# Kernel optimization log

Measured on AMD Instinct MI355X. Metric: run time of the kernel, lower is better.

Reference implementation:

```python
import jax, jax.numpy as jnp
import numpy as np

BN_EPS = 1e-5
LN_EPS = 1e-5

N_NODES = 50000
N_EDGES = 800000
D_IN = 128
D_HID = 512


def _batchnorm(h, gamma, beta):
    # training-mode BatchNorm1d: biased variance over the node/batch dim
    m = jnp.mean(h, axis=0)
    v = jnp.mean(jnp.square(h - m), axis=0)
    return (h - m) * jax.lax.rsqrt(v + BN_EPS) * gamma + beta


def setup_inputs() -> dict:
    key = jax.random.key(0)
    ks = jax.random.split(key, 8)
    x = jax.random.normal(ks[0], (N_NODES, D_IN), dtype=jnp.float32)
    edge_index = jax.random.randint(ks[1], (2, N_EDGES), 0, N_NODES, dtype=jnp.int64)
    s1 = 1.0 / np.sqrt(D_IN)
    s2 = 1.0 / np.sqrt(D_HID)
    W1 = jax.random.uniform(ks[2], (D_IN, D_HID), jnp.float32, -s1, s1)
    b1 = jax.random.uniform(ks[3], (D_HID,), jnp.float32, -s1, s1)
    W2 = jax.random.uniform(ks[4], (D_HID, D_IN), jnp.float32, -s2, s2)
    b2 = jax.random.uniform(ks[5], (D_IN,), jnp.float32, -s2, s2)
    return {
        "x": x,
        "edge_index": edge_index,
        "W1": W1, "b1": b1,
        "bn1_g": jnp.ones((D_HID,), jnp.float32), "bn1_b": jnp.zeros((D_HID,), jnp.float32),
        "W2": W2, "b2": b2,
        "bn2_g": jnp.ones((D_IN,), jnp.float32), "bn2_b": jnp.zeros((D_IN,), jnp.float32),
        "ln_g": jnp.ones((D_IN,), jnp.float32), "ln_b": jnp.zeros((D_IN,), jnp.float32),
    }


def reference(x, edge_index, W1, b1, bn1_g, bn1_b, W2, b2, bn2_g, bn2_b, ln_g, ln_b):
    n = x.shape[0]
    src = edge_index[0]
    dst = edge_index[1]
    # GIN aggregation: sum of neighbor (source) features at each destination node
    agg = jax.ops.segment_sum(x[src], dst, num_segments=n)  # [N, D_IN]
    h = x + agg  # (1 + eps) * x + agg, eps = 0
    # MLP: Linear -> BN -> ReLU -> Linear -> BN -> ReLU (final activation)
    h = jax.nn.relu(_batchnorm(h @ W1 + b1, bn1_g, bn1_b))  # [N, D_HID]
    h = jax.nn.relu(_batchnorm(h @ W2 + b2, bn2_g, bn2_b))  # [N, D_IN]
    # residual + LayerNorm (dropout p=0 -> identity)
    out = h + x
    m = jnp.mean(out, axis=-1, keepdims=True)
    v = jnp.mean(jnp.square(out - m), axis=-1, keepdims=True)
    out = (out - m) * jax.lax.rsqrt(v + LN_EPS) * ln_g + ln_b
    return out
```

## Files before the change

kernel.cpp:

```cpp
#include <hip/hip_runtime.h>
#include <stdint.h>

#define N_NODES 50000
#define N_EDGES 800000
#define D_IN    128
#define D_HID   512
#define NPAD    50048
#define NTILES  391
#define SCAN_NB 196
#define G_TILES 782
#define G_BLOCKS 256
#define H1_FULL_NEED 64797440LL

typedef __attribute__((ext_vector_type(8))) short short8;
typedef __attribute__((ext_vector_type(4))) float f32x4;

__device__ __forceinline__ float bf2f(unsigned short u) {
    union { unsigned int i; float f; } v; v.i = ((unsigned int)u) << 16; return v.f;
}
__device__ __forceinline__ unsigned short f2bf(float f) {
    union { float f; unsigned int i; } v; v.f = f;
    unsigned int r = v.i + 0x7fffu + ((v.i >> 16) & 1u);
    return (unsigned short)(r >> 16);
}
__device__ __forceinline__ float loadP(const void* p, long i, int isf) {
    return isf ? ((const float*)p)[i] : bf2f(((const unsigned short*)p)[i]);
}

__global__ void k_init(const void* __restrict__ x, const int* __restrict__ ei,
                       float* __restrict__ stats, int* __restrict__ counts,
                       int* __restrict__ flags) {
    int t = threadIdx.x;
    if (blockIdx.x < 201) {
        int i = blockIdx.x * 256 + t;
        if (i < 1408) stats[i] = 0.f;
        else if (i < 1408 + N_NODES) counts[i - 1408] = 0;
    } else {
        __shared__ int sh[2];
        if (t == 0) { sh[0] = 0; sh[1] = 1; }
        __syncthreads();
        const unsigned short* xu = (const unsigned short*)x;
        for (int i = t; i < 8192; i += 256)
            if (((xu[i] >> 7) & 0xFF) == 0xFF) sh[0] = 1;
        for (int k = t; k < 64; k += 256)
            if (ei[2 * k + 1] != 0) sh[1] = 0;
        __syncthreads();
        if (t == 0) { flags[0] = sh[0]; flags[1] = sh[1]; }
    }
}

__global__ void k_transpose2(const void* __restrict__ W1, const void* __restrict__ W2,
                             unsigned short* __restrict__ w1t, unsigned short* __restrict__ w2t,
                             const int* __restrict__ flags) {
    int isf = flags[0];
    int idx = blockIdx.x * 256 + threadIdx.x;
    if (idx < D_IN * D_HID) {
        int n = idx >> 7, k = idx & 127;
        int src = k * D_HID + n;
        w1t[idx] = isf ? f2bf(((const float*)W1)[src])
                       : ((const unsigned short*)W1)[src];
    } else {
        int j = idx - D_IN * D_HID;
        int n = j >> 9, k = j & 511;
        int src = k * D_IN + n;
        w2t[j] = isf ? f2bf(((const float*)W2)[src])
                     : ((const unsigned short*)W2)[src];
    }
}

__global__ void k_count(const int* __restrict__ ei, int* __restrict__ counts,
                        const int* __restrict__ flags) {
    int i64 = flags[1];
    int e = blockIdx.x * 256 + threadIdx.x;
    int d = i64 ? ei[2 * N_EDGES + 2 * e] : ei[N_EDGES + e];
    d = min(max(d, 0), N_NODES - 1);
    atomicAdd(&counts[d], 1);
}

__global__ __launch_bounds__(256) void k_scan_block(const int* __restrict__ counts,
                                                    int* __restrict__ rowptr,
                                                    int* __restrict__ partials) {
    __shared__ int a[256], b[256];
    int t = threadIdx.x;
    int idx = blockIdx.x * 256 + t;
    int c = (idx < N_NODES) ? counts[idx] : 0;
    a[t] = c;
    __syncthreads();
    int* src = a; int* dst = b;
    for (int off = 1; off < 256; off <<= 1) {
        dst[t] = src[t] + ((t >= off) ? src[t - off] : 0);
        __syncthreads();
        int* tmp = src; src = dst; dst = tmp;
    }
    if (idx < N_NODES) rowptr[idx] = src[t] - c;
    if (t == 255) partials[blockIdx.x] = src[255];
}

__global__ __launch_bounds__(256) void k_scan_part(int* __restrict__ partials) {
    __shared__ int a[256], b[256];
    int t = threadIdx.x;
    int c = (t < SCAN_NB) ? partials[t] : 0;
    a[t] = c;
    __syncthreads();
    int* src = a; int* dst = b;
    for (int off = 1; off < 256; off <<= 1) {
        dst[t] = src[t] + ((t >= off) ? src[t - off] : 0);
        __syncthreads();
        int* tmp = src; src = dst; dst = tmp;
    }
    if (t < SCAN_NB) partials[t] = src[t] - c;
}

__global__ void k_scan_add(int* __restrict__ rowptr, int* __restrict__ cursor,
                           const int* __restrict__ partials) {
    int idx = blockIdx.x * 256 + threadIdx.x;
    if (idx < N_NODES) {
        int v = rowptr[idx] + partials[blockIdx.x];
        rowptr[idx] = v;
        cursor[idx] = v;
    } else if (idx == N_NODES) {
        rowptr[N_NODES] = N_EDGES;
    }
}

__global__ void k_fill(const int* __restrict__ ei, int* __restrict__ cursor,
                       int* __restrict__ bucket, const int* __restrict__ flags) {
    int i64 = flags[1];
    int e = blockIdx.x * 256 + threadIdx.x;
    int s, d;
    if (i64) { s = ei[2 * e]; d = ei[2 * N_EDGES + 2 * e]; }
    else     { s = ei[e];     d = ei[N_EDGES + e]; }
    s = min(max(s, 0), N_NODES - 1);
    d = min(max(d, 0), N_NODES - 1);
    int pos = atomicAdd(&cursor[d], 1);
    bucket[pos] = s;
}

__global__ __launch_bounds__(256) void k_gather(const int* __restrict__ rowptr,
                                                const int* __restrict__ bucket,
                                                const void* __restrict__ x,
                                                unsigned short* __restrict__ agg,
                                                const int* __restrict__ flags) {
    int isf = flags[0];
    int w = threadIdx.x >> 6, lane = threadIdx.x & 63;
    int row = blockIdx.x * 4 + w;
    float a0 = 0.f, a1 = 0.f;
    if (row < N_NODES) {
        int beg = rowptr[row], end = rowptr[row + 1];
        if (isf) {
            const float* xf = (const float*)x;
            float2 v = *(const float2*)(xf + (size_t)row * D_IN + lane * 2);
            a0 = v.x; a1 = v.y;
            int j = beg;
            for (; j + 8 <= end; j += 8) {
                float2 n0 = *(const float2*)(xf + (size_t)bucket[j] * D_IN + lane * 2);
                float2 n1 = *(const float2*)(xf + (size_t)bucket[j + 1] * D_IN + lane * 2);
                float2 n2 = *(const float2*)(xf + (size_t)bucket[j + 2] * D_IN + lane * 2);
                float2 n3 = *(const float2*)(xf + (size_t)bucket[j + 3] * D_IN + lane * 2);
                float2 n4 = *(const float2*)(xf + (size_t)bucket[j + 4] * D_IN + lane * 2);
                float2 n5 = *(const float2*)(xf + (size_t)bucket[j + 5] * D_IN + lane * 2);
                float2 n6 = *(const float2*)(xf + (size_t)bucket[j + 6] * D_IN + lane * 2);
                float2 n7 = *(const float2*)(xf + (size_t)bucket[j + 7] * D_IN + lane * 2);
                a0 += ((n0.x + n1.x) + (n2.x + n3.x)) + ((n4.x + n5.x) + (n6.x + n7.x));
                a1 += ((n0.y + n1.y) + (n2.y + n3.y)) + ((n4.y + n5.y) + (n6.y + n7.y));
            }
            for (; j + 4 <= end; j += 4) {
                float2 n0 = *(const float2*)(xf + (size_t)bucket[j] * D_IN + lane * 2);
                float2 n1 = *(const float2*)(xf + (size_t)bucket[j + 1] * D_IN + lane * 2);
                float2 n2 = *(const float2*)(xf + (size_t)bucket[j + 2] * D_IN + lane * 2);
                float2 n3 = *(const float2*)(xf + (size_t)bucket[j + 3] * D_IN + lane * 2);
                a0 += (n0.x + n1.x) + (n2.x + n3.x);
                a1 += (n0.y + n1.y) + (n2.y + n3.y);
            }
            for (; j < end; j++) {
                float2 n = *(const float2*)(xf + (size_t)bucket[j] * D_IN + lane * 2);
                a0 += n.x; a1 += n.y;
            }
        } else {
            const unsigned int* xu = (const unsigned int*)x;
            unsigned int u = xu[(size_t)row * 64 + lane];
            a0 = bf2f(u & 0xffff); a1 = bf2f(u >> 16);
            int j = beg;
            for (; j + 8 <= end; j += 8) {
                unsigned int u0 = xu[(size_t)bucket[j] * 64 + lane];
                unsigned int u1 = xu[(size_t)bucket[j + 1] * 64 + lane];
                unsigned int u2 = xu[(size_t)bucket[j + 2] * 64 + lane];
                unsigned int u3 = xu[(size_t)bucket[j + 3] * 64 + lane];
                unsigned int u4 = xu[(size_t)bucket[j + 4] * 64 + lane];
                unsigned int u5 = xu[(size_t)bucket[j + 5] * 64 + lane];
                unsigned int u6 = xu[(size_t)bucket[j + 6] * 64 + lane];
                unsigned int u7 = xu[(size_t)bucket[j + 7] * 64 + lane];
                a0 += ((bf2f(u0 & 0xffff) + bf2f(u1 & 0xffff)) + (bf2f(u2 & 0xffff) + bf2f(u3 & 0xffff)))
                    + ((bf2f(u4 & 0xffff) + bf2f(u5 & 0xffff)) + (bf2f(u6 & 0xffff) + bf2f(u7 & 0xffff)));
                a1 += ((bf2f(u0 >> 16) + bf2f(u1 >> 16)) + (bf2f(u2 >> 16) + bf2f(u3 >> 16)))
                    + ((bf2f(u4 >> 16) + bf2f(u5 >> 16)) + (bf2f(u6 >> 16) + bf2f(u7 >> 16)));
            }
            for (; j + 4 <= end; j += 4) {
                unsigned int u0 = xu[(size_t)bucket[j] * 64 + lane];
                unsigned int u1 = xu[(size_t)bucket[j + 1] * 64 + lane];
                unsigned int u2 = xu[(size_t)bucket[j + 2] * 64 + lane];
                unsigned int u3 = xu[(size_t)bucket[j + 3] * 64 + lane];
                a0 += (bf2f(u0 & 0xffff) + bf2f(u1 & 0xffff)) + (bf2f(u2 & 0xffff) + bf2f(u3 & 0xffff));
                a1 += (bf2f(u0 >> 16) + bf2f(u1 >> 16)) + (bf2f(u2 >> 16) + bf2f(u3 >> 16));
            }
            for (; j < end; j++) {
                unsigned int n = xu[(size_t)bucket[j] * 64 + lane];
                a0 += bf2f(n & 0xffff); a1 += bf2f(n >> 16);
            }
        }
    }
    unsigned int o = (unsigned int)f2bf(a0) | ((unsigned int)f2bf(a1) << 16);
    ((unsigned int*)agg)[(size_t)row * 64 + lane] = o;
}

__global__ __launch_bounds__(256) void k_gram(const unsigned short* __restrict__ aggb,
                                              float* __restrict__ Gpart,
                                              float* __restrict__ colsum) {
    __shared__ unsigned short ldsT[128 * 64];
    int t = threadIdx.x;
    int wid = t >> 6, lane = t & 63;
    int wm = wid & 1, wn = wid >> 1;
    int quad = lane >> 4, l16 = lane & 15;
    f32x4 acc[4][4] = {};
    float cs = 0.f;
    int cscol = t & 127, cskh = t >> 7;
    for (int tile = blockIdx.x; tile < G_TILES; tile += G_BLOCKS) {
        __syncthreads();
        size_t rowbase = (size_t)tile * 64;
#pragma unroll
        for (int jj = 0; jj < 2; jj++) {
            int j = t + jj * 256;
            int c = j >> 5, rp = j & 31;
            uint4 v0 = *(const uint4*)(aggb + (rowbase + 2 * rp) * 128 + c * 8);
            uint4 v1 = *(const uint4*)(aggb + (rowbase + 2 * rp + 1) * 128 + c * 8);
            const unsigned short* p0 = (const unsigned short*)&v0;
            const unsigned short* p1 = (const unsigned short*)&v1;
            int k = 2 * rp, kc = k >> 3, ko = k & 7;
#pragma unroll
            for (int e = 0; e < 8; e++) {
                int col = c * 8 + e;
                *(unsigned int*)(ldsT + col * 64 + ((kc ^ (col & 7)) * 8) + ko) =
                    (unsigned int)p0[e] | ((unsigned int)p1[e] << 16);
            }
        }
        __syncthreads();
#pragma unroll
        for (int ksub = 0; ksub < 2; ksub++) {
            short8 fa[4], fb[4];
#pragma unroll
            for (int mt = 0; mt < 4; mt++) {
                int col = wm * 64 + mt * 16 + l16;
                fa[mt] = *(const short8*)(ldsT + col * 64 + (((ksub * 4 + quad) ^ (col & 7)) * 8));
            }
#pragma unroll
            for (int nt = 0; nt < 4; nt++) {
                int col = wn * 64 + nt * 16 + l16;
                fb[nt] = *(const short8*)(ldsT + col * 64 + (((ksub * 4 + quad) ^ (col & 7)) * 8));
            }
#pragma unroll
            for (int mt = 0; mt < 4; mt++)
#pragma unroll
                for (int nt = 0; nt < 4; nt++)
                    acc[mt][nt] = __builtin_amdgcn_mfma_f32_16x16x32_bf16(fa[mt], fb[nt], acc[mt][nt], 0, 0, 0);
        }
#pragma unroll
        for (int kc = 0; kc < 4; kc++) {
            short8 v = *(const short8*)(ldsT + cscol * 64 + (((cskh * 4 + kc) ^ (cscol & 7)) * 8));
#pragma unroll
            for (int e = 0; e < 8; e++) cs += bf2f((unsigned short)v[e]);
        }
    }
    float* gp = Gpart + (size_t)blockIdx.x * 16384;
#pragma unroll
    for (int mt = 0; mt < 4; mt++)
#pragma unroll
        for (int nt = 0; nt < 4; nt++) {
            int m = wm * 64 + mt * 16 + quad * 4;
            int n = wn * 64 + nt * 16 + l16;
#pragma unroll
            for (int rg = 0; rg < 4; rg++)
                gp[(m + rg) * 128 + n] = acc[mt][nt][rg];
        }
    atomicAdd(&colsum[cscol], cs);
}

__global__ void k_gred(const float* __restrict__ Gpart, float* __restrict__ G) {
    int i = blockIdx.x * 256 + threadIdx.x;
    float s = 0.f;
#pragma unroll 8
    for (int b = 0; b < G_BLOCKS; b++) s += Gpart[(size_t)b * 16384 + i];
    G[i] = s;
}

__global__ __launch_bounds__(256) void k_bn1(const float* __restrict__ G,
                                             const float* __restrict__ colsum,
                                             const unsigned short* __restrict__ w1t,
                                             const void* __restrict__ b1,
                                             float* __restrict__ sum1,
                                             float* __restrict__ sumsq1,
                                             const int* __restrict__ flags) {
    int isf = flags[0];
    __shared__ float wsh[4][128];
    int t = threadIdx.x, wid = t >> 6, lane = t & 63;
    int n = blockIdx.x * 4 + wid;
    unsigned int u = *(const unsigned int*)(w1t + (size_t)n * 128 + lane * 2);
    wsh[wid][lane * 2] = bf2f(u & 0xffff);
    wsh[wid][lane * 2 + 1] = bf2f(u >> 16);
    __syncthreads();
    const float* w = wsh[wid];
    const f32x4* g0 = (const f32x4*)(G + (size_t)lane * 128);
    const f32x4* g1 = (const f32x4*)(G + (size_t)(lane + 64) * 128);
    float t0 = 0.f, t1 = 0.f;
#pragma unroll 4
    for (int q4 = 0; q4 < 32; q4++) {
        f32x4 a = g0[q4], b = g1[q4];
        float w0 = w[q4 * 4], w1 = w[q4 * 4 + 1], w2 = w[q4 * 4 + 2], w3 = w[q4 * 4 + 3];
        t0 += a[0] * w0 + a[1] * w1 + a[2] * w2 + a[3] * w3;
        t1 += b[0] * w0 + b[1] * w1 + b[2] * w2 + b[3] * w3;
    }
    float sq = w[lane] * t0 + w[lane + 64] * t1;
    float s  = w[lane] * colsum[lane] + w[lane + 64] * colsum[lane + 64];
#pragma unroll
    for (int m = 1; m < 64; m <<= 1) {
        sq += __shfl_xor(sq, m, 64);
        s  += __shfl_xor(s, m, 64);
    }
    if (lane == 0) {
        float b = loadP(b1, n, isf);
        sum1[n]   = s + (float)N_NODES * b;
        sumsq1[n] = sq + 2.f * b * s + (float)N_NODES * b * b;
    }
}

__global__ __launch_bounds__(256, 2) void k_mlp1(const unsigned short* __restrict__ aggc,
                                                 const unsigned short* __restrict__ w1t,
                                                 const void* __restrict__ b1,
                                                 const void* __restrict__ g1,
                                                 const void* __restrict__ bb1,
                                                 const float* __restrict__ sum1,
                                                 const float* __restrict__ sumsq1,
                                                 unsigned short* __restrict__ h1c,
                                                 const int* __restrict__ flags) {
    __shared__ unsigned short bufA[128 * 128];
    __shared__ unsigned short bufW[128 * 128];
    int isf = flags[0];
    int t = threadIdx.x;
    int m0 = (blockIdx.x >> 2) * 128;
    int nb = blockIdx.x & 3;
    int r = t >> 1, half = t & 1;
    int wid = t >> 6, lane = t & 63;
    int wm = wid & 1, wn = wid >> 1;
    int quad = lane >> 4, l16 = lane & 15;
#pragma unroll
    for (int i = 0; i < 8; i++) {
        int chunk = half * 8 + i;
        int sw = ((chunk ^ (r & 15)) * 8);
        *(uint4*)(bufA + r * 128 + sw) = *(const uint4*)(aggc + (size_t)(m0 + r) * 128 + chunk * 8);
        *(uint4*)(bufW + r * 128 + sw) = *(const uint4*)(w1t + (size_t)(nb * 128 + r) * 128 + chunk * 8);
    }
    __syncthreads();
    f32x4 acc[4][4] = {};
#pragma unroll
    for (int ks = 0; ks < 4; ks++) {
        short8 af[4], bw[4];
#pragma unroll
        for (int mt = 0; mt < 4; mt++)
            af[mt] = *(const short8*)(bufA + (wm * 64 + mt * 16 + l16) * 128 + (((ks * 4 + quad) ^ l16) * 8));
#pragma unroll
        for (int nt = 0; nt < 4; nt++)
            bw[nt] = *(const short8*)(bufW + (wn * 64 + nt * 16 + l16) * 128 + (((ks * 4 + quad) ^ l16) * 8));
#pragma unroll
        for (int mt = 0; mt < 4; mt++)
#pragma unroll
            for (int nt = 0; nt < 4; nt++)
                acc[mt][nt] = __builtin_amdgcn_mfma_f32_16x16x32_bf16(af[mt], bw[nt], acc[mt][nt], 0, 0, 0);
    }
    __syncthreads();
#pragma unroll
    for (int nt = 0; nt < 4; nt++) {
        int nl = wn * 64 + nt * 16 + l16;
        int n1 = nb * 128 + nl;
        float mz = sum1[n1] * (1.f / N_NODES);
        float vz = sumsq1[n1] * (1.f / N_NODES) - mz * mz;
        float inv = rsqrtf(fmaxf(vz, 0.f) + 1e-5f);
        float A = loadP(g1, n1, isf) * inv;
        float C = loadP(bb1, n1, isf) - mz * A + loadP(b1, n1, isf) * A;
        int ccw = nl >> 3, cl = nl & 7;
#pragma unroll
        for (int mt = 0; mt < 4; mt++)
#pragma unroll
            for (int rg = 0; rg < 4; rg++) {
                int R = wm * 64 + mt * 16 + quad * 4 + rg;
                bufA[R * 128 + ((ccw ^ (R & 15)) * 8) + cl] = f2bf(fmaxf(acc[mt][nt][rg] * A + C, 0.f));
            }
    }
    __syncthreads();
#pragma unroll
    for (int i = 0; i < 8; i++) {
        int idx = t + i * 256;
        int rr = idx >> 4, chunk = idx & 15;
        *(uint4*)(h1c + (size_t)(m0 + rr) * D_HID + nb * 128 + chunk * 8) =
            *(const uint4*)(bufA + rr * 128 + ((chunk ^ (rr & 15)) * 8));
    }
}

__global__ __launch_bounds__(256, 2) void k_mlp1r(const unsigned short* __restrict__ aggb,
                                                  const unsigned short* __restrict__ w1t,
                                                  const void* __restrict__ b1,
                                                  unsigned short* __restrict__ h1,
                                                  float* __restrict__ sum1,
                                                  float* __restrict__ sumsq1,
                                                  const int* __restrict__ flags) {
    __shared__ unsigned short bufA[128 * 128];
    __shared__ unsigned short bufW[128 * 128];
    __shared__ float sred[256];
    int isf = flags[0];
    int t = threadIdx.x;
    int m0 = (blockIdx.x >> 2) * 128;
    int nb = blockIdx.x & 3;
    int r = t >> 1, half = t & 1;
    int wid = t >> 6, lane = t & 63;
    int wm = wid & 1, wn = wid >> 1;
    int quad = lane >> 4, l16 = lane & 15;
    sred[t] = 0.f;
#pragma unroll
    for (int i = 0; i < 8; i++) {
        int chunk = half * 8 + i;
        int sw = ((chunk ^ (r & 15)) * 8);
        *(uint4*)(bufA + r * 128 + sw) = *(const uint4*)(aggb + (size_t)(m0 + r) * 128 + chunk * 8);
        *(uint4*)(bufW + r * 128 + sw) = *(const uint4*)(w1t + (size_t)(nb * 128 + r) * 128 + chunk * 8);
    }
    __syncthreads();
    f32x4 acc[4][4] = {};
#pragma unroll
    for (int ks = 0; ks < 4; ks++) {
        short8 af[4], bw[4];
#pragma unroll
        for (int mt = 0; mt < 4; mt++)
            af[mt] = *(const short8*)(bufA + (wm * 64 + mt * 16 + l16) * 128 + (((ks * 4 + quad) ^ l16) * 8));
#pragma unroll
        for (int nt = 0; nt < 4; nt++)
            bw[nt] = *(const short8*)(bufW + (wn * 64 + nt * 16 + l16) * 128 + (((ks * 4 + quad) ^ l16) * 8));
#pragma unroll
        for (int mt = 0; mt < 4; mt++)
#pragma unroll
            for (int nt = 0; nt < 4; nt++)
                acc[mt][nt] = __builtin_amdgcn_mfma_f32_16x16x32_bf16(af[mt], bw[nt], acc[mt][nt], 0, 0, 0);
    }
    __syncthreads();
#pragma unroll
    for (int nt = 0; nt < 4; nt++) {
        int nl = wn * 64 + nt * 16 + l16;
        int n1 = nb * 128 + nl;
        float bias = loadP(b1, n1, isf);
        int ccw = nl >> 3, cl = nl & 7;
        float s = 0.f, ss = 0.f;
#pragma unroll
        for (int mt = 0; mt < 4; mt++)
#pragma unroll
            for (int rg = 0; rg < 4; rg++) {
                int R = wm * 64 + mt * 16 + quad * 4 + rg;
                float z = acc[mt][nt][rg] + bias;
                bufA[R * 128 + ((ccw ^ (R & 15)) * 8) + cl] = f2bf(z);
                if (m0 + R < N_NODES) { s += z; ss += z * z; }
            }
        s += __shfl_xor(s, 16, 64); ss += __shfl_xor(ss, 16, 64);
        s += __shfl_xor(s, 32, 64); ss += __shfl_xor(ss, 32, 64);
        if (quad == 0) { atomicAdd(&sred[nl], s); atomicAdd(&sred[128 + nl], ss); }
    }
    __syncthreads();
#pragma unroll
    for (int i = 0; i < 8; i++) {
        int idx = t + i * 256;
        int rr = idx >> 4, chunk = idx & 15;
        *(uint4*)(h1 + (size_t)(m0 + rr) * D_HID + nb * 128 + chunk * 8) =
            *(const uint4*)(bufA + rr * 128 + ((chunk ^ (rr & 15)) * 8));
    }
    if (t < 128)      atomicAdd(&sum1[nb * 128 + t], sred[t]);
    else              atomicAdd(&sumsq1[nb * 128 + (t - 128)], sred[t]);
}

__global__ __launch_bounds__(256, 3) void k_mlp2(const unsigned short* __restrict__ h1c,
                                                 const unsigned short* __restrict__ w2t,
                                                 const void* __restrict__ b2,
                                                 unsigned short* __restrict__ h2c,
                                                 float* __restrict__ sum2,
                                                 float* __restrict__ sumsq2,
                                                 const int* __restrict__ flags,
                                                 int roff) {
    __shared__ unsigned short bufA[64 * 128];
    __shared__ unsigned short bufW[128 * 128];
    __shared__ float sred[256];
    int isf = flags[0];
    int t = threadIdx.x;
    int m0 = blockIdx.x * 64;
    int rw = t >> 1, halfw = t & 1;
    int wid = t >> 6, lane = t & 63;
    int wm = wid & 1, wn = wid >> 1;
    int quad = lane >> 4, l16 = lane & 15;
    sred[t] = 0.f;
    f32x4 acc[2][4] = {};
    for (int kb = 0; kb < 4; kb++) {
        __syncthreads();
#pragma unroll
        for (int i = 0; i < 4; i++) {
            int idx = t + i * 256;
            int rr = idx >> 4, chunk = idx & 15;
            *(uint4*)(bufA + rr * 128 + ((chunk ^ (rr & 15)) * 8)) =
                *(const uint4*)(h1c + (size_t)(m0 + rr) * D_HID + kb * 128 + chunk * 8);
        }
#pragma unroll
        for (int i = 0; i < 8; i++) {
            int chunk = halfw * 8 + i;
            *(uint4*)(bufW + rw * 128 + ((chunk ^ (rw & 15)) * 8)) =
                *(const uint4*)(w2t + (size_t)rw * D_HID + kb * 128 + chunk * 8);
        }
        __syncthreads();
#pragma unroll
        for (int ks = 0; ks < 4; ks++) {
            short8 af[2], bw[4];
#pragma unroll
            for (int mt = 0; mt < 2; mt++)
                af[mt] = *(const short8*)(bufA + (wm * 32 + mt * 16 + l16) * 128 + (((ks * 4 + quad) ^ l16) * 8));
#pragma unroll
            for (int nt = 0; nt < 4; nt++)
                bw[nt] = *(const short8*)(bufW + (wn * 64 + nt * 16 + l16) * 128 + (((ks * 4 + quad) ^ l16) * 8));
#pragma unroll
            for (int mt = 0; mt < 2; mt++)
#pragma unroll
                for (int nt = 0; nt < 4; nt++)
                    acc[mt][nt] = __builtin_amdgcn_mfma_f32_16x16x32_bf16(af[mt], bw[nt], acc[mt][nt], 0, 0, 0);
        }
    }
    __syncthreads();
#pragma unroll
    for (int nt = 0; nt < 4; nt++) {
        int n = wn * 64 + nt * 16 + l16;
        float bias = loadP(b2, n, isf);
        float s = 0.f, ss = 0.f;
#pragma unroll
        for (int mt = 0; mt < 2; mt++) {
            int Rl = wm * 32 + mt * 16 + quad * 4;
#pragma unroll
            for (int rg = 0; rg < 4; rg++) {
                float z = acc[mt][nt][rg] + bias;
                bufW[(Rl + rg) * 128 + n] = f2bf(z);
                if (roff + m0 + Rl + rg < N_NODES) { s += z; ss += z * z; }
            }
        }
        s += __shfl_xor(s, 16, 64); ss += __shfl_xor(ss, 16, 64);
        s += __shfl_xor(s, 32, 64); ss += __shfl_xor(ss, 32, 64);
        if (quad == 0) { atomicAdd(&sred[n], s); atomicAdd(&sred[128 + n], ss); }
    }
    __syncthreads();
#pragma unroll
    for (int i = 0; i < 4; i++) {
        int idx = t + i * 256;
        int rr = idx >> 4, seg = idx & 15;
        *(uint4*)(h2c + (size_t)(m0 + rr) * D_IN + seg * 8) = *(const uint4*)(bufW + rr * 128 + seg * 8);
    }
    {
        int n = t & 127;
        if (t < 128) atomicAdd(&sum2[n], sred[n]);
        else         atomicAdd(&sumsq2[n], sred[128 + n]);
    }
}

__global__ __launch_bounds__(256, 3) void k_mlp2b(const unsigned short* __restrict__ h1,
                                                  const unsigned short* __restrict__ w2t,
                                                  const void* __restrict__ b2,
                                                  const void* __restrict__ g1,
                                                  const void* __restrict__ bb1,
                                                  const float* __restrict__ sum1,
                                                  const float* __restrict__ sumsq1,
                                                  unsigned short* __restrict__ h2,
                                                  float* __restrict__ sum2,
                                                  float* __restrict__ sumsq2,
                                                  const int* __restrict__ flags) {
    __shared__ unsigned short bufA[64 * 128];
    __shared__ unsigned short bufW[128 * 128];
    __shared__ float sred[256];
    __shared__ float bnA[512], bnC[512];
    int isf = flags[0];
    int t = threadIdx.x;
    int m0 = blockIdx.x * 64;
    int rw = t >> 1, halfw = t & 1;
    int wid = t >> 6, lane = t & 63;
    int wm = wid & 1, wn = wid >> 1;
    int quad = lane >> 4, l16 = lane & 15;
    sred[t] = 0.f;
    for (int i = t; i < 512; i += 256) {
        float mz = sum1[i] * (1.f / N_NODES);
        float vz = sumsq1[i] * (1.f / N_NODES) - mz * mz;
        float inv = rsqrtf(fmaxf(vz, 0.f) + 1e-5f);
        float A = loadP(g1, i, isf) * inv;
        bnA[i] = A;
        bnC[i] = loadP(bb1, i, isf) - mz * A;
    }
    f32x4 acc[2][4] = {};
    for (int kb = 0; kb < 4; kb++) {
        __syncthreads();
#pragma unroll
        for (int i = 0; i < 4; i++) {
            int idx = t + i * 256;
            int rr = idx >> 4, chunk = idx & 15;
            uint4 v = *(const uint4*)(h1 + (size_t)(m0 + rr) * D_HID + kb * 128 + chunk * 8);
            const unsigned short* pv = (const unsigned short*)&v;
            unsigned short o[8];
            int cb = kb * 128 + chunk * 8;
#pragma unroll
            for (int e = 0; e < 8; e++)
                o[e] = f2bf(fmaxf(bf2f(pv[e]) * bnA[cb + e] + bnC[cb + e], 0.f));
            *(uint4*)(bufA + rr * 128 + ((chunk ^ (rr & 15)) * 8)) = *(const uint4*)o;
        }
#pragma unroll
        for (int i = 0; i < 8; i++) {
            int chunk = halfw * 8 + i;
            *(uint4*)(bufW + rw * 128 + ((chunk ^ (rw & 15)) * 8)) =
                *(const uint4*)(w2t + (size_t)rw * D_HID + kb * 128 + chunk * 8);
        }
        __syncthreads();
#pragma unroll
        for (int ks = 0; ks < 4; ks++) {
            short8 af[2], bw[4];
#pragma unroll
            for (int mt = 0; mt < 2; mt++)
                af[mt] = *(const short8*)(bufA + (wm * 32 + mt * 16 + l16) * 128 + (((ks * 4 + quad) ^ l16) * 8));
#pragma unroll
            for (int nt = 0; nt < 4; nt++)
                bw[nt] = *(const short8*)(bufW + (wn * 64 + nt * 16 + l16) * 128 + (((ks * 4 + quad) ^ l16) * 8));
#pragma unroll
            for (int mt = 0; mt < 2; mt++)
#pragma unroll
                for (int nt = 0; nt < 4; nt++)
                    acc[mt][nt] = __builtin_amdgcn_mfma_f32_16x16x32_bf16(af[mt], bw[nt], acc[mt][nt], 0, 0, 0);
        }
    }
    __syncthreads();
#pragma unroll
    for (int nt = 0; nt < 4; nt++) {
        int n = wn * 64 + nt * 16 + l16;
        float bias = loadP(b2, n, isf);
        float s = 0.f, ss = 0.f;
#pragma unroll
        for (int mt = 0; mt < 2; mt++) {
            int Rl = wm * 32 + mt * 16 + quad * 4;
#pragma unroll
            for (int rg = 0; rg < 4; rg++) {
                float z = acc[mt][nt][rg] + bias;
                bufW[(Rl + rg) * 128 + n] = f2bf(z);
                if (m0 + Rl + rg < N_NODES) { s += z; ss += z * z; }
            }
        }
        s += __shfl_xor(s, 16, 64); ss += __shfl_xor(ss, 16, 64);
        s += __shfl_xor(s, 32, 64); ss += __shfl_xor(ss, 32, 64);
        if (quad == 0) { atomicAdd(&sred[n], s); atomicAdd(&sred[128 + n], ss); }
    }
    __syncthreads();
#pragma unroll
    for (int i = 0; i < 4; i++) {
        int idx = t + i * 256;
        int rr = idx >> 4, seg = idx & 15;
        *(uint4*)(h2 + (size_t)(m0 + rr) * D_IN + seg * 8) = *(const uint4*)(bufW + rr * 128 + seg * 8);
    }
    {
        int n = t & 127;
        if (t < 128) atomicAdd(&sum2[n], sred[n]);
        else         atomicAdd(&sumsq2[n], sred[128 + n]);
    }
}

__global__ __launch_bounds__(256) void k_final(const unsigned short* __restrict__ h2,
                                               const void* __restrict__ x,
                                               const float* __restrict__ sum2,
                                               const float* __restrict__ sumsq2,
                                               const void* __restrict__ g2,
                                               const void* __restrict__ bb2,
                                               const void* __restrict__ lng,
                                               const void* __restrict__ lnb,
                                               void* __restrict__ out,
                                               const int* __restrict__ flags) {
    int isf = flags[0];
    __shared__ float a2s[D_IN], c2s[D_IN];
    int t = threadIdx.x;
    if (t < D_IN) {
        float m = sum2[t] * (1.f / N_NODES);
        float v = sumsq2[t] * (1.f / N_NODES) - m * m;
        float inv = rsqrtf(fmaxf(v, 0.f) + 1e-5f);
        float a = loadP(g2, t, isf) * inv;
        a2s[t] = a;
        c2s[t] = loadP(bb2, t, isf) - m * a;
    }
    __syncthreads();
    int w = t >> 6, lane = t & 63;
    int row = blockIdx.x * 4 + w;
    if (row >= N_NODES) return;
    size_t base = (size_t)row * D_IN;
    int c0 = lane * 2, c1 = lane * 2 + 1;
    unsigned int hu = ((const unsigned int*)h2)[base / 2 + lane];
    float x0, x1;
    if (isf) {
        float2 xv = *((const float2*)x + base / 2 + lane);
        x0 = xv.x; x1 = xv.y;
    } else {
        unsigned int xu = ((const unsigned int*)x)[base / 2 + lane];
        x0 = bf2f(xu & 0xffff); x1 = bf2f(xu >> 16);
    }
    float o0 = fmaxf(a2s[c0] * bf2f(hu & 0xffff) + c2s[c0], 0.f) + x0;
    float o1 = fmaxf(a2s[c1] * bf2f(hu >> 16) + c2s[c1], 0.f) + x1;
    float s = o0 + o1, ss = o0 * o0 + o1 * o1;
#pragma unroll
    for (int m = 1; m < 64; m <<= 1) {
        s += __shfl_xor(s, m, 64);
        ss += __shfl_xor(ss, m, 64);
    }
    float mean = s * (1.f / D_IN);
    float var = ss * (1.f / D_IN) - mean * mean;
    float inv = rsqrtf(fmaxf(var, 0.f) + 1e-5f);
    float r0 = (o0 - mean) * inv * loadP(lng, c0, isf) + loadP(lnb, c0, isf);
    float r1 = (o1 - mean) * inv * loadP(lng, c1, isf) + loadP(lnb, c1, isf);
    if (isf) {
        *((float2*)out + base / 2 + lane) = make_float2(r0, r1);
    } else {
        ((unsigned int*)out)[base / 2 + lane] = (unsigned int)f2bf(r0) | ((unsigned int)f2bf(r1) << 16);
    }
}

extern "C" void kernel_launch(void* const* d_in, const int* in_sizes, int n_in,
                              void* d_out, int out_size, void* d_ws, size_t ws_size,
                              hipStream_t stream) {
    const void* x    = d_in[0];
    const int*  ei   = (const int*)d_in[1];
    const void* W1   = d_in[2];
    const void* b1   = d_in[3];
    const void* bn1g = d_in[4];
    const void* bn1b = d_in[5];
    const void* W2   = d_in[6];
    const void* b2   = d_in[7];
    const void* bn2g = d_in[8];
    const void* bn2b = d_in[9];
    const void* lng  = d_in[10];
    const void* lnb  = d_in[11];

    char* ws = (char*)d_ws;
    float* stats   = (float*)ws;
    float* sum1    = stats;
    float* sumsq1  = stats + 512;
    float* sum2    = stats + 1024;
    float* sumsq2  = stats + 1152;
    float* colsum  = stats + 1280;
    int*   flags   = (int*)(ws + 5632);
    int*   partials= (int*)(ws + 5696);
    int*   rowptr  = (int*)(ws + 8192);
    int*   cursor  = (int*)(ws + 208256);
    unsigned short* w1t = (unsigned short*)(ws + 408320);
    unsigned short* w2t = (unsigned short*)(ws + 539392);
    float* G       = (float*)(ws + 670464);
    unsigned short* agg = (unsigned short*)(ws + 736000);
    unsigned short* h2  = agg;
    int*   bucket  = (int*)(ws + 13548288);
    float* Gpart   = (float*)(ws + 16748288);
    unsigned short* h1r = (unsigned short*)(ws + 13548288);

    k_init<<<202, 256, 0, stream>>>(x, ei, stats, cursor, flags);
    k_transpose2<<<512, 256, 0, stream>>>(W1, W2, w1t, w2t, flags);
    k_count<<<N_EDGES / 256, 256, 0, stream>>>(ei, cursor, flags);
    k_scan_block<<<SCAN_NB, 256, 0, stream>>>(cursor, rowptr, partials);
    k_scan_part<<<1, 256, 0, stream>>>(partials);
    k_scan_add<<<SCAN_NB, 256, 0, stream>>>(rowptr, cursor, partials);
    k_fill<<<N_EDGES / 256, 256, 0, stream>>>(ei, cursor, bucket, flags);
    k_gather<<<NPAD / 4, 256, 0, stream>>>(rowptr, bucket, x, agg, flags);

    if ((long long)ws_size >= H1_FULL_NEED) {
        k_mlp1r<<<NTILES * 4, 256, 0, stream>>>(agg, w1t, b1, h1r, sum1, sumsq1, flags);
        k_mlp2b<<<NPAD / 64, 256, 0, stream>>>(h1r, w2t, b2, bn1g, bn1b, sum1, sumsq1,
                                               h2, sum2, sumsq2, flags);
    } else {
        k_gram<<<G_BLOCKS, 256, 0, stream>>>(agg, Gpart, colsum);
        k_gred<<<64, 256, 0, stream>>>(Gpart, G);
        k_bn1<<<128, 256, 0, stream>>>(G, colsum, w1t, b1, sum1, sumsq1, flags);
        long long avail = (long long)ws_size - 13548288LL;
        int max_tiles = (avail > 0) ? (int)(avail / 131072LL) : 1;
        if (max_tiles < 1)  max_tiles = 1;
        if (max_tiles > NTILES) max_tiles = NTILES;
        int nch = (NTILES + max_tiles - 1) / max_tiles;
        int per = (NTILES + nch - 1) / nch;
        for (int done = 0; done < NTILES; done += per) {
            int nt = NTILES - done;
            if (nt > per) nt = per;
            const unsigned short* aggc = agg + (size_t)done * 128 * 128;
            unsigned short* h2c = h2 + (size_t)done * 128 * 128;
            k_mlp1<<<nt * 4, 256, 0, stream>>>(aggc, w1t, b1, bn1g, bn1b, sum1, sumsq1, h1r, flags);
            k_mlp2<<<nt * 2, 256, 0, stream>>>(h1r, w2t, b2, h2c, sum2, sumsq2, flags, done * 128);
        }
    }

    k_final<<<(N_NODES + 3) / 4, 256, 0, stream>>>(h2, x, sum2, sumsq2, bn2g, bn2b, lng, lnb, d_out, flags);
}
```

Before: 362.8 us.

## Double k_mlp2b row tile to 128 with 512-thread blocks

Restructures the second MLP GEMM kernel so each block handles 128 rows with 8 waves instead of 64 rows with 4 waves. Each W2 slice loaded into shared memory is reused across twice as many rows. BN1 scale and shift are read as vectors once per k-block instead of per element. The cost is larger shared memory per block, fewer blocks (391 on the device) and possible load imbalance or lower occupancy.

```diff
diff --git a/kernel.cpp b/kernel.cpp
--- a/kernel.cpp
+++ b/kernel.cpp
@@ -566,7 +566,7 @@
     }
 }
 
-__global__ __launch_bounds__(256, 3) void k_mlp2b(const unsigned short* __restrict__ h1,
+__global__ __launch_bounds__(512, 4) void k_mlp2b(const unsigned short* __restrict__ h1,
                                                   const unsigned short* __restrict__ w2t,
                                                   const void* __restrict__ b2,
                                                   const void* __restrict__ g1,
@@ -577,47 +577,57 @@
                                                   float* __restrict__ sum2,
                                                   float* __restrict__ sumsq2,
                                                   const int* __restrict__ flags) {
-    __shared__ unsigned short bufA[64 * 128];
+    __shared__ unsigned short bufA[128 * 128];
     __shared__ unsigned short bufW[128 * 128];
     __shared__ float sred[256];
-    __shared__ float bnA[512], bnC[512];
+    __shared__ __align__(16) float bnA[512];
+    __shared__ __align__(16) float bnC[512];
     int isf = flags[0];
     int t = threadIdx.x;
-    int m0 = blockIdx.x * 64;
-    int rw = t >> 1, halfw = t & 1;
+    int m0 = blockIdx.x * 128;
     int wid = t >> 6, lane = t & 63;
-    int wm = wid & 1, wn = wid >> 1;
+    int wm = wid & 3, wn = wid >> 2;
     int quad = lane >> 4, l16 = lane & 15;
-    sred[t] = 0.f;
-    for (int i = t; i < 512; i += 256) {
-        float mz = sum1[i] * (1.f / N_NODES);
-        float vz = sumsq1[i] * (1.f / N_NODES) - mz * mz;
+    int chunkT = t & 15;
+    if (t < 256) sred[t] = 0.f;
+    if (t < 512) {
+        float mz = sum1[t] * (1.f / N_NODES);
+        float vz = sumsq1[t] * (1.f / N_NODES) - mz * mz;
         float inv = rsqrtf(fmaxf(vz, 0.f) + 1e-5f);
-        float A = loadP(g1, i, isf) * inv;
-        bnA[i] = A;
-        bnC[i] = loadP(bb1, i, isf) - mz * A;
+        float A = loadP(g1, t, isf) * inv;
+        bnA[t] = A;
+        bnC[t] = loadP(bb1, t, isf) - mz * A;
     }
     f32x4 acc[2][4] = {};
     for (int kb = 0; kb < 4; kb++) {
         __syncthreads();
+        f32x4 A0 = *(const f32x4*)(bnA + kb * 128 + chunkT * 8);
+        f32x4 A1 = *(const f32x4*)(bnA + kb * 128 + chunkT * 8 + 4);
+        f32x4 C0 = *(const f32x4*)(bnC + kb * 128 + chunkT * 8);
+        f32x4 C1 = *(const f32x4*)(bnC + kb * 128 + chunkT * 8 + 4);
 #pragma unroll
         for (int i = 0; i < 4; i++) {
-            int idx = t + i * 256;
-            int rr = idx >> 4, chunk = idx & 15;
-            uint4 v = *(const uint4*)(h1 + (size_t)(m0 + rr) * D_HID + kb * 128 + chunk * 8);
+            int idx = t + i * 512;
+            int rr = idx >> 4;
+            uint4 v = *(const uint4*)(h1 + (size_t)(m0 + rr) * D_HID + kb * 128 + chunkT * 8);
             const unsigned short* pv = (const unsigned short*)&v;
             unsigned short o[8];
-            int cb = kb * 128 + chunk * 8;
-#pragma unroll
-            for (int e = 0; e < 8; e++)
-                o[e] = f2bf(fmaxf(bf2f(pv[e]) * bnA[cb + e] + bnC[cb + e], 0.f));
-            *(uint4*)(bufA + rr * 128 + ((chunk ^ (rr & 15)) * 8)) = *(const uint4*)o;
-        }
-#pragma unroll
-        for (int i = 0; i < 8; i++) {
-            int chunk = halfw * 8 + i;
-            *(uint4*)(bufW + rw * 128 + ((chunk ^ (rw & 15)) * 8)) =
-                *(const uint4*)(w2t + (size_t)rw * D_HID + kb * 128 + chunk * 8);
+            o[0] = f2bf(fmaxf(bf2f(pv[0]) * A0[0] + C0[0], 0.f));
+            o[1] = f2bf(fmaxf(bf2f(pv[1]) * A0[1] + C0[1], 0.f));
+            o[2] = f2bf(fmaxf(bf2f(pv[2]) * A0[2] + C0[2], 0.f));
+            o[3] = f2bf(fmaxf(bf2f(pv[3]) * A0[3] + C0[3], 0.f));
+            o[4] = f2bf(fmaxf(bf2f(pv[4]) * A1[0] + C1[0], 0.f));
+            o[5] = f2bf(fmaxf(bf2f(pv[5]) * A1[1] + C1[1], 0.f));
+            o[6] = f2bf(fmaxf(bf2f(pv[6]) * A1[2] + C1[2], 0.f));
+            o[7] = f2bf(fmaxf(bf2f(pv[7]) * A1[3] + C1[3], 0.f));
+            *(uint4*)(bufA + rr * 128 + ((chunkT ^ (rr & 15)) * 8)) = *(const uint4*)o;
+        }
+#pragma unroll
+        for (int i = 0; i < 4; i++) {
+            int idx = t + i * 512;
+            int rr = idx >> 4;
+            *(uint4*)(bufW + rr * 128 + ((chunkT ^ (rr & 15)) * 8)) =
+                *(const uint4*)(w2t + (size_t)rr * D_HID + kb * 128 + chunkT * 8);
         }
         __syncthreads();
 #pragma unroll
@@ -659,11 +669,11 @@
     __syncthreads();
 #pragma unroll
     for (int i = 0; i < 4; i++) {
-        int idx = t + i * 256;
+        int idx = t + i * 512;
         int rr = idx >> 4, seg = idx & 15;
         *(uint4*)(h2 + (size_t)(m0 + rr) * D_IN + seg * 8) = *(const uint4*)(bufW + rr * 128 + seg * 8);
     }
-    {
+    if (t < 256) {
         int n = t & 127;
         if (t < 128) atomicAdd(&sum2[n], sred[n]);
         else         atomicAdd(&sumsq2[n], sred[128 + n]);
@@ -773,8 +783,8 @@
 
     if ((long long)ws_size >= H1_FULL_NEED) {
         k_mlp1r<<<NTILES * 4, 256, 0, stream>>>(agg, w1t, b1, h1r, sum1, sumsq1, flags);
-        k_mlp2b<<<NPAD / 64, 256, 0, stream>>>(h1r, w2t, b2, bn1g, bn1b, sum1, sumsq1,
-                                               h2, sum2, sumsq2, flags);
+        k_mlp2b<<<NTILES, 512, 0, stream>>>(h1r, w2t, b2, bn1g, bn1b, sum1, sumsq1,
+                                            h2, sum2, sumsq2, flags);
     } else {
         k_gram<<<G_BLOCKS, 256, 0, stream>>>(agg, Gpart, colsum);
         k_gred<<<64, 256, 0, stream>>>(Gpart, G);
```

After: 339.3 us. 1.07x faster.
